# Kernel optimization log

Measured on AMD Instinct MI355X. Metric: run time of the kernel, lower is better.

## Reference

```python
import jax, jax.numpy as jnp
import numpy as np

B, C, H, W = 4, 1024, 14, 14
L = 80          # num labels / graph nodes
WD = 300        # word embedding dim
INTER = 1024    # semantic intermediary dim
OUT = 2048      # output_dim
TIME_STEP = 3


def setup_inputs() -> dict:
    key = jax.random.key(0)
    ks = jax.random.split(key, 24)
    s = 0.02  # weight scale to keep gates/tanh in sane range
    return {
        "img_feature_map": jax.random.normal(ks[0], (B, C, H, W), jnp.float32),
        "word_embedding": jax.random.normal(ks[1], (L, WD), jnp.float32),
        "adjacency": jax.random.uniform(ks[2], (L, L), jnp.float32) / L,
        "fc1_w": jax.random.normal(ks[3], (INTER, C), jnp.float32) * s,
        "fc2_w": jax.random.normal(ks[4], (INTER, WD), jnp.float32) * s,
        "fc3_w": jax.random.normal(ks[5], (INTER, INTER), jnp.float32) * s,
        "fc3_b": jnp.zeros((INTER,), jnp.float32),
        "fca_w": jax.random.normal(ks[6], (1, INTER), jnp.float32) * s,
        "fca_b": jnp.zeros((1,), jnp.float32),
        "w3": jax.random.normal(ks[7], (C, 2 * C), jnp.float32) * s,
        "b3": jnp.zeros((C,), jnp.float32),
        "u3": jax.random.normal(ks[8], (C, C), jnp.float32) * s,
        "u3b": jnp.zeros((C,), jnp.float32),
        "w4": jax.random.normal(ks[9], (C, 2 * C), jnp.float32) * s,
        "b4": jnp.zeros((C,), jnp.float32),
        "w5": jax.random.normal(ks[10], (C, 2 * C), jnp.float32) * s,
        "b5": jnp.zeros((C,), jnp.float32),
        "u5": jax.random.normal(ks[11], (C, C), jnp.float32) * s,
        "u5b": jnp.zeros((C,), jnp.float32),
        "fco_w": jax.random.normal(ks[12], (OUT, 2 * C), jnp.float32) * s,
        "fco_b": jnp.zeros((OUT,), jnp.float32),
    }


def _semantic(fmap, word_emb, fc1_w, fc2_w, fc3_w, fc3_b, fca_w, fca_b):
    # Faithful to torch: view(-1, C) on a contiguous (B,C,H,W) tensor is a raw
    # row-major reinterpret (NOT a BHWC transpose). jnp.reshape matches.
    b, c, h, w = fmap.shape
    x = fmap.reshape(-1, c)                                   # (B*H*W, C)
    f_wh = x @ fc1_w.T                                        # (N, INTER)
    f_wd = word_emb @ fc2_w.T                                 # (L, INTER)
    lb = jnp.tanh(f_wh[:, None, :] * f_wd[None, :, :])        # (N, L, INTER)
    lb = lb @ fc3_w.T + fc3_b                                 # (N, L, INTER)
    coeff = lb @ fca_w.T + fca_b                              # (N, L, 1)
    coeff = coeff.reshape(b, L, h * w)                        # torch .view semantics
    coeff = jax.nn.softmax(coeff, axis=2)
    coeff = coeff.reshape(b, h, w, L)
    fmap_bhwc = fmap.reshape(b, h, w, c)                      # raw reinterpret, as torch
    return jnp.einsum('bhwl,bhwc->blc', coeff, fmap_bhwc)     # (B, L, C)


def _ggnn(nodes, adj, w3, b3, u3, u3b, w4, b4, w5, b5, u5, u5b):
    for _ in range(TIME_STEP):
        a = jnp.einsum('nm,bmd->bnd', adj, nodes)             # in == out matrix
        av = jnp.concatenate([a, a], axis=-1)                 # (B, L, 2C)
        u3x = nodes @ u3.T + u3b
        z = jax.nn.sigmoid(av @ w3.T + b3 + u3x)
        r = jax.nn.sigmoid(av @ w4.T + b4 + u3x)              # torch bug: reuses fc_eq3_u
        hcand = jnp.tanh(av @ w5.T + b5 + (r * nodes) @ u5.T + u5b)
        nodes = (1.0 - z) * nodes + z * hcand
    return nodes


def reference(img_feature_map, word_embedding, adjacency,
              fc1_w, fc2_w, fc3_w, fc3_b, fca_w, fca_b,
              w3, b3, u3, u3b, w4, b4, w5, b5, u5, u5b,
              fco_w, fco_b):
    g = _semantic(img_feature_map, word_embedding,
                  fc1_w, fc2_w, fc3_w, fc3_b, fca_w, fca_b)   # (B, L, C)
    nodes = _ggnn(g, adjacency, w3, b3, u3, u3b, w4, b4, w5, b5, u5, u5b)
    feat = jnp.concatenate([nodes, g], axis=-1)               # (B, L, 2C)
    out = jnp.tanh(feat @ fco_w.T + fco_b)                    # (B, L, OUT)
    return out
```

## Files before the change

### kernel.cpp

```cpp
#include <hip/hip_runtime.h>
#include <hip/hip_bf16.h>

#define LL 80
#define NPIX 784
#define PBATCH 15680

#define DI __device__ __forceinline__

typedef short s8v __attribute__((ext_vector_type(8)));
typedef short short4v __attribute__((ext_vector_type(4)));
typedef float f32x4 __attribute__((ext_vector_type(4)));

DI float b2f(__hip_bfloat16 x) { return __bfloat162float(x); }
DI float s2f(short h) { return __uint_as_float(((unsigned int)(unsigned short)h) << 16); }

DI short f2b(float x) {
    unsigned int b = __float_as_uint(x);
    b += 0x7fffu + ((b >> 16) & 1u);
    return (short)(b >> 16);
}

template <int F> DI float LD(const void* p, int i) {
    if (F) return ((const float*)p)[i];
    return b2f(((const __hip_bfloat16*)p)[i]);
}
DI float LDf(int f, const void* p, int i) { return f ? ((const float*)p)[i] : b2f(((const __hip_bfloat16*)p)[i]); }

DI float fast_tanh(float x) {
    float e = __expf(2.0f * x);
    return 1.0f - 2.0f / (e + 1.0f);
}
DI float fast_sigmoid(float x) { return 1.0f / (1.0f + __expf(-x)); }

__global__ __launch_bounds__(256) void detect_dtype(const void* probe, int n, int* flag) {
    __shared__ int bad;
    if (threadIdx.x == 0) bad = 0;
    __syncthreads();
    int c = 0;
    for (int i = threadIdx.x; i < n; i += 256) {
        float v = b2f(((const __hip_bfloat16*)probe)[i]);
        if (!(fabsf(v) < 1000.0f)) c++;
    }
    if (c) atomicAdd(&bad, c);
    __syncthreads();
    if (threadIdx.x == 0) *flag = (bad > 8) ? 1 : 0;
}

DI void cvt_part(int f, const void* src, short* __restrict__ dst, int blk, int n) {
    int i0 = (blk * 256 + threadIdx.x) * 4;
    if (i0 >= n) return;
    if (f) {
        float4 v = *(const float4*)((const float*)src + i0);
        short4v o = { f2b(v.x), f2b(v.y), f2b(v.z), f2b(v.w) };
        *(short4v*)(dst + i0) = o;
    } else {
        *(short4v*)(dst + i0) = *(const short4v*)((const short*)src + i0);
    }
}

DI void wcat_part(int f, const void* w3, const void* w4, const void* w5, const void* u3,
                  short* __restrict__ wcat, int blk) {
    int i0 = (blk * 256 + threadIdx.x) * 4;
    int nr = i0 >> 10, k = i0 & 1023;
    int j = nr >> 10, r = nr & 1023;
    const void* W = (j == 0) ? w3 : (j == 1) ? w4 : (j == 2) ? w5 : u3;
    float4 v;
    if (j < 3) {
        if (f) {
            float4 x = *(const float4*)((const float*)W + r * 2048 + k);
            float4 y = *(const float4*)((const float*)W + r * 2048 + 1024 + k);
            v.x = x.x + y.x; v.y = x.y + y.y; v.z = x.z + y.z; v.w = x.w + y.w;
        } else {
            const short* Ws = (const short*)W;
            short4v x = *(const short4v*)(Ws + r * 2048 + k);
            short4v y = *(const short4v*)(Ws + r * 2048 + 1024 + k);
            v.x = s2f(x.x) + s2f(y.x); v.y = s2f(x.y) + s2f(y.y);
            v.z = s2f(x.z) + s2f(y.z); v.w = s2f(x.w) + s2f(y.w);
        }
    } else {
        if (f) v = *(const float4*)((const float*)W + r * 1024 + k);
        else {
            short4v x = *(const short4v*)((const short*)W + r * 1024 + k);
            v.x = s2f(x.x); v.y = s2f(x.y); v.z = s2f(x.z); v.w = s2f(x.w);
        }
    }
    short4v o = { f2b(v.x), f2b(v.y), f2b(v.z), f2b(v.w) };
    *(short4v*)(wcat + i0) = o;
}

template <int F>
DI void u_part(const void* fc3_w, const void* fca_w, float* __restrict__ uP, int jsplit) {
    int k4 = threadIdx.x * 4;
    float4 acc = {0.f, 0.f, 0.f, 0.f};
    for (int j = jsplit * 16; j < jsplit * 16 + 16; j++) {
        float fa = LD<F>(fca_w, j);
        float4 row;
        if (F) row = *(const float4*)((const float*)fc3_w + j * 1024 + k4);
        else {
            short4v x = *(const short4v*)((const short*)fc3_w + j * 1024 + k4);
            row.x = s2f(x.x); row.y = s2f(x.y); row.z = s2f(x.z); row.w = s2f(x.w);
        }
        acc.x += fa * row.x; acc.y += fa * row.y;
        acc.z += fa * row.z; acc.w += fa * row.w;
    }
    *(float4*)(uP + jsplit * 1024 + k4) = acc;
}

template <int F>
DI void c0_part(const void* fc3_b, const void* fca_w, const void* fca_b,
                float* c0, float* red) {
    float acc = 0.f;
    for (int j = threadIdx.x; j < 1024; j += 256)
        acc += LD<F>(fc3_b, j) * LD<F>(fca_w, j);
    red[threadIdx.x] = acc;
    __syncthreads();
    for (int s = 128; s > 0; s >>= 1) {
        if (threadIdx.x < s) red[threadIdx.x] += red[threadIdx.x + s];
        __syncthreads();
    }
    if (threadIdx.x == 0) *c0 = red[0] + LD<F>(fca_b, 0);
}

template <int F>
DI void fc2_part(float* lds, const void* word, const void* fc2_w, float* C,
                 int bx, int by, int kb, int ke) {
    float* As = lds;
    float* Ws2 = lds + 1088;
    const int tid = threadIdx.x;
    const int tx = tid & 15, ty = tid >> 4;
    const int m0 = by * 64, n0 = bx * 64;
    const int M = 80;
    float acc[4][4] = {};

    for (int k0 = kb; k0 < ke; k0 += 16) {
#pragma unroll
        for (int i = 0; i < 4; i++) {
            int idx = tid + i * 256;
            int kk = idx & 15, mm = idx >> 4;
            int m = m0 + mm, k = k0 + kk;
            As[kk * 68 + mm] = (m < M && k < ke) ? LD<F>(word, m * 300 + k) : 0.f;
        }
#pragma unroll
        for (int i = 0; i < 4; i++) {
            int idx = tid + i * 256;
            int kk = idx & 15, nn = idx >> 4;
            int n = n0 + nn, k = k0 + kk;
            Ws2[kk * 68 + nn] = (k < ke) ? LD<F>(fc2_w, n * 300 + k) : 0.f;
        }
        __syncthreads();
#pragma unroll
        for (int kk = 0; kk < 16; kk++) {
            float4 av = *(const float4*)(&As[kk * 68 + ty * 4]);
            float4 wv = *(const float4*)(&Ws2[kk * 68 + tx * 4]);
            float a4[4] = {av.x, av.y, av.z, av.w};
            float w4[4] = {wv.x, wv.y, wv.z, wv.w};
#pragma unroll
            for (int i = 0; i < 4; i++)
#pragma unroll
                for (int j = 0; j < 4; j++)
                    acc[i][j] += a4[i] * w4[j];
        }
        __syncthreads();
    }

    for (int i = 0; i < 4; i++) {
        int m = m0 + ty * 4 + i;
        if (m >= M) continue;
        for (int j = 0; j < 4; j++)
            C[m * 1024 + n0 + tx * 4 + j] = acc[i][j];
    }
}

__global__ __launch_bounds__(256) void mega_prep(
    const int* flag,
    const void* fmap, const void* fc1_w, const void* u5w, const void* fco_w,
    const void* w3, const void* w4, const void* w5, const void* u3,
    const void* fc3_w, const void* fc3_b, const void* fca_w, const void* fca_b,
    const void* word, const void* fc2_w,
    short* fmap_b, short* fc1w_b, short* u5w_b, short* wcat_b, short* fcow_b,
    float* uP, float* c0, float* f_wdP) {
    __shared__ float lds[2176];
    int f = *flag;
    int bid = blockIdx.x;
    if (bid < 64) {
        if (f) u_part<1>(fc3_w, fca_w, uP, bid);
        else   u_part<0>(fc3_w, fca_w, uP, bid);
    } else if (bid == 64) {
        if (f) c0_part<1>(fc3_b, fca_w, fca_b, c0, lds);
        else   c0_part<0>(fc3_b, fca_w, fca_b, c0, lds);
    } else if (bid < 193) {
        int r = bid - 65;
        int sp = r >> 5, rr = r & 31;
        int kb = sp * 80, ke = (sp == 3) ? 300 : kb + 80;
        float* C = f_wdP + sp * 81920;
        if (f) fc2_part<1>(lds, word, fc2_w, C, rr & 15, rr >> 4, kb, ke);
        else   fc2_part<0>(lds, word, fc2_w, C, rr & 15, rr >> 4, kb, ke);
    }
    else if (bid < 977)  cvt_part(f, fmap,  fmap_b, bid - 193,  802816);
    else if (bid < 2001) cvt_part(f, fc1_w, fc1w_b, bid - 977,  1048576);
    else if (bid < 3025) cvt_part(f, u5w,   u5w_b,  bid - 2001, 1048576);
    else if (bid < 7121) wcat_part(f, w3, w4, w5, u3, wcat_b, bid - 3025);
    else                 cvt_part(f, fco_w, fcow_b, bid - 7121, 4194304);
}

__global__ __launch_bounds__(256) void reduce_pre(
    const float* __restrict__ uP, const float* __restrict__ f_wdP,
    float* __restrict__ u, float* __restrict__ f_wd) {
    if (blockIdx.x < 80) {
        int i4 = (blockIdx.x * 256 + threadIdx.x) * 4;
        float4 a = *(const float4*)(f_wdP + i4);
        float4 b = *(const float4*)(f_wdP + 81920 + i4);
        float4 c = *(const float4*)(f_wdP + 163840 + i4);
        float4 d = *(const float4*)(f_wdP + 245760 + i4);
        float4 o = {a.x+b.x+c.x+d.x, a.y+b.y+c.y+d.y, a.z+b.z+c.z+d.z, a.w+b.w+c.w+d.w};
        *(float4*)(f_wd + i4) = o;
    } else {
        int k4 = threadIdx.x * 4;
        float4 acc = {0.f, 0.f, 0.f, 0.f};
        for (int p = 0; p < 64; p++) {
            float4 q = *(const float4*)(uP + p * 1024 + k4);
            acc.x += q.x; acc.y += q.y; acc.z += q.z; acc.w += q.w;
        }
        *(float4*)(u + k4) = acc;
    }
}

DI void mcore_b(const short* __restrict__ A, int lda,
                const short* __restrict__ B, int ldb,
                float* __restrict__ C, int ldc,
                int M, int kb, int ke, int m0, int n0) {
    __shared__ short As[4][64][8];
    __shared__ short Ws[4][64][8];
    const int tid = threadIdx.x;
    const int wv = tid >> 6, lane = tid & 63;
    const int mA = tid & 63, qA = tid >> 6;
    const int gm = m0 + mA;
    const int lp = (mA & 15) | (qA << 4), lg = mA >> 4;
    f32x4 acc[4] = {};

    s8v va = {0,0,0,0,0,0,0,0};
    if (gm < M) va = *(const s8v*)(A + gm * lda + kb + 8 * qA);
    s8v vb = *(const s8v*)(B + (n0 + mA) * ldb + kb + 8 * qA);

    for (int k0 = kb; k0 < ke; k0 += 32) {
        *(s8v*)&As[lg][lp][0] = va;
        *(s8v*)&Ws[lg][lp][0] = vb;
        __syncthreads();
        int kn = k0 + 32;
        if (kn < ke) {
            if (gm < M) va = *(const s8v*)(A + gm * lda + kn + 8 * qA);
            vb = *(const s8v*)(B + (n0 + mA) * ldb + kn + 8 * qA);
        }
        s8v af = *(const s8v*)&As[wv][lane][0];
#pragma unroll
        for (int nf = 0; nf < 4; nf++) {
            s8v bf = *(const s8v*)&Ws[nf][lane][0];
            acc[nf] = __builtin_amdgcn_mfma_f32_16x16x32_bf16(af, bf, acc[nf], 0, 0, 0);
        }
        __syncthreads();
    }

    const int q = lane >> 4, cc = lane & 15;
#pragma unroll
    for (int nf = 0; nf < 4; nf++) {
        int n = n0 + 16 * nf + cc;
#pragma unroll
        for (int r = 0; r < 4; r++) {
            int m = m0 + 16 * wv + q * 4 + r;
            if (m < M) C[m * ldc + n] = acc[nf][r];
        }
    }
}

__global__ __launch_bounds__(256) void mfma_fc1(
    const short* __restrict__ fmap_b, const short* __restrict__ fc1w_b,
    float* __restrict__ fhP) {
    int z = blockIdx.z;
    mcore_b(fmap_b, 1024, fc1w_b, 1024, fhP + z * 802816, 1024,
            NPIX, z * 512, z * 512 + 512, blockIdx.y * 64, blockIdx.x * 64);
}

__global__ __launch_bounds__(256) void mfma_gate(
    const short* __restrict__ a_b, const short* __restrict__ nodes_b,
    const short* __restrict__ wcat_b, float* __restrict__ gP) {
    int z = blockIdx.z;
    const short* A = (blockIdx.x >= 48) ? nodes_b : a_b;
    mcore_b(A, 1024, wcat_b, 1024, gP + z * 1310720, 4096,
            320, z * 512, z * 512 + 512, blockIdx.y * 64, blockIdx.x * 64);
}

__global__ __launch_bounds__(256) void mfma_u5f(
    const int* flag, const short* __restrict__ rn_b, const short* __restrict__ u5w_b,
    const float* __restrict__ gP,
    const void* b3, const void* u3b, const void* b5, const void* u5b,
    float* __restrict__ nodes, short* __restrict__ nodes_b) {
    __shared__ short As[4][64][8];
    __shared__ short Ws[4][64][8];
    const int tid = threadIdx.x;
    const int wv = tid >> 6, lane = tid & 63;
    const int mA = tid & 63, qA = tid >> 6;
    const int lp = (mA & 15) | (qA << 4), lg = mA >> 4;
    const int m0 = blockIdx.y * 64, n0 = blockIdx.x * 64;
    f32x4 acc[4] = {};

    s8v va = *(const s8v*)(rn_b + (m0 + mA) * 1024 + 8 * qA);
    s8v vb = *(const s8v*)(u5w_b + (n0 + mA) * 1024 + 8 * qA);

    for (int k0 = 0; k0 < 1024; k0 += 32) {
        *(s8v*)&As[lg][lp][0] = va;
        *(s8v*)&Ws[lg][lp][0] = vb;
        __syncthreads();
        int kn = k0 + 32;
        if (kn < 1024) {
            va = *(const s8v*)(rn_b + (m0 + mA) * 1024 + kn + 8 * qA);
            vb = *(const s8v*)(u5w_b + (n0 + mA) * 1024 + kn + 8 * qA);
        }
        s8v af = *(const s8v*)&As[wv][lane][0];
#pragma unroll
        for (int nf = 0; nf < 4; nf++) {
            s8v bf = *(const s8v*)&Ws[nf][lane][0];
            acc[nf] = __builtin_amdgcn_mfma_f32_16x16x32_bf16(af, bf, acc[nf], 0, 0, 0);
        }
        __syncthreads();
    }

    const int f = *flag;
    const int q = lane >> 4, cc = lane & 15;
#pragma unroll
    for (int nf = 0; nf < 4; nf++) {
        int n = n0 + 16 * nf + cc;
        float bb3 = LDf(f, b3, n), bu3 = LDf(f, u3b, n);
        float bb5 = LDf(f, b5, n), bu5 = LDf(f, u5b, n);
#pragma unroll
        for (int r = 0; r < 4; r++) {
            int m = m0 + 16 * wv + q * 4 + r;
            int i = m * 1024 + n, base = m * 4096;
            float az = gP[base + n]        + gP[1310720 + base + n];
            float ah = gP[base + 2048 + n] + gP[1310720 + base + 2048 + n];
            float ux = gP[base + 3072 + n] + gP[1310720 + base + 3072 + n];
            float z = fast_sigmoid(az + ux + bb3 + bu3);
            float h = fast_tanh(ah + acc[nf][r] + bb5 + bu5);
            float nd = (1.f - z) * nodes[i] + z * h;
            nodes[i] = nd;
            nodes_b[i] = f2b(nd);
        }
    }
}

__global__ __launch_bounds__(256) void mfma_finf(
    const int* flag, const short* __restrict__ nodes_b, const short* __restrict__ g_b,
    const short* __restrict__ fcow_b, const void* fco_b, void* out) {
    __shared__ short As[4][64][8];
    __shared__ short Ws[4][64][8];
    const int tid = threadIdx.x;
    const int wv = tid >> 6, lane = tid & 63;
    const int mA = tid & 63, qA = tid >> 6;
    const int lp = (mA & 15) | (qA << 4), lg = mA >> 4;
    const int m0 = blockIdx.y * 64, n0 = blockIdx.x * 64;
    f32x4 acc[4] = {};

    s8v va = *(const s8v*)(nodes_b + (m0 + mA) * 1024 + 8 * qA);
    s8v vb = *(const s8v*)(fcow_b + (n0 + mA) * 2048 + 8 * qA);

    for (int k0 = 0; k0 < 2048; k0 += 32) {
        *(s8v*)&As[lg][lp][0] = va;
        *(s8v*)&Ws[lg][lp][0] = vb;
        __syncthreads();
        int kn = k0 + 32;
        if (kn < 2048) {
            const short* Apn = (kn < 1024) ? nodes_b : (g_b - 1024);
            va = *(const s8v*)(Apn + (m0 + mA) * 1024 + kn + 8 * qA);
            vb = *(const s8v*)(fcow_b + (n0 + mA) * 2048 + kn + 8 * qA);
        }
        s8v af = *(const s8v*)&As[wv][lane][0];
#pragma unroll
        for (int nf = 0; nf < 4; nf++) {
            s8v bf = *(const s8v*)&Ws[nf][lane][0];
            acc[nf] = __builtin_amdgcn_mfma_f32_16x16x32_bf16(af, bf, acc[nf], 0, 0, 0);
        }
        __syncthreads();
    }

    const int f = *flag;
    const int q = lane >> 4, cc = lane & 15;
#pragma unroll
    for (int nf = 0; nf < 4; nf++) {
        int n = n0 + 16 * nf + cc;
        float bias = LDf(f, fco_b, n);
#pragma unroll
        for (int r = 0; r < 4; r++) {
            int m = m0 + 16 * wv + q * 4 + r;
            float v = fast_tanh(acc[nf][r] + bias);
            if (f) ((float*)out)[m * 2048 + n] = v;
            else   ((__hip_bfloat16*)out)[m * 2048 + n] = __float2bfloat16(v);
        }
    }
}

__global__ __launch_bounds__(256) void coeff_kernel(
    const float* __restrict__ fhP, const float* __restrict__ f_wd,
    const float* __restrict__ u, const float* __restrict__ c0p,
    float* __restrict__ s) {
    int n = blockIdx.x;
    __shared__ float4 fh4[256];
    __shared__ float4 uu4[256];
    int t = threadIdx.x;
    {
        float4 a0 = *(const float4*)(fhP + n * 1024 + t * 4);
        float4 a1 = *(const float4*)(fhP + 802816 + n * 1024 + t * 4);
        float4 fv = {a0.x + a1.x, a0.y + a1.y, a0.z + a1.z, a0.w + a1.w};
        fh4[t] = fv;
        uu4[t] = *(const float4*)(u + t * 4);
    }
    __syncthreads();
    float c0 = *c0p;
    int wave = t >> 6, lane = t & 63;
    int b = n / 196, hw = n % 196;
    int l0 = blockIdx.y * 40;
    for (int l = l0 + wave; l < l0 + 40; l += 4) {
        const float4* fd4 = (const float4*)(f_wd + l * 1024);
        float p = 0.f;
#pragma unroll
        for (int k = 0; k < 4; k++) {
            int idx = lane + k * 64;
            float4 h = fh4[idx];
            float4 d = fd4[idx];
            float4 uu = uu4[idx];
            p += fast_tanh(h.x * d.x) * uu.x;
            p += fast_tanh(h.y * d.y) * uu.y;
            p += fast_tanh(h.z * d.z) * uu.z;
            p += fast_tanh(h.w * d.w) * uu.w;
        }
        for (int off = 32; off > 0; off >>= 1) p += __shfl_down(p, off);
        if (lane == 0) s[b * PBATCH + hw * LL + l] = p + c0;
    }
}

__global__ __launch_bounds__(64) void softmax196(float* __restrict__ s) {
    float* p = s + blockIdx.x * 196;
    int lane = threadIdx.x;
    float v[4];
    float mx = -1e30f;
#pragma unroll
    for (int i = 0; i < 4; i++) {
        int idx = lane + i * 64;
        v[i] = (idx < 196) ? p[idx] : -1e30f;
        mx = fmaxf(mx, v[i]);
    }
    for (int off = 32; off > 0; off >>= 1) mx = fmaxf(mx, __shfl_down(mx, off));
    mx = __shfl(mx, 0);
    float sum = 0.f;
#pragma unroll
    for (int i = 0; i < 4; i++) {
        int idx = lane + i * 64;
        if (idx < 196) { v[i] = __expf(v[i] - mx); sum += v[i]; }
    }
    for (int off = 32; off > 0; off >>= 1) sum += __shfl_down(sum, off);
    sum = __shfl(sum, 0);
    float inv = 1.f / sum;
#pragma unroll
    for (int i = 0; i < 4; i++) {
        int idx = lane + i * 64;
        if (idx < 196) p[idx] = v[i] * inv;
    }
}

__global__ __launch_bounds__(256) void g_kernel(
    const float* __restrict__ s, const short* __restrict__ fmap_b,
    float* __restrict__ nodes, short* __restrict__ nodes_b, short* __restrict__ g_b) {
    int bl = blockIdx.x;
    int b = bl / LL, l = bl % LL;
    __shared__ float co[196];
    for (int i = threadIdx.x; i < 196; i += 256)
        co[i] = s[b * PBATCH + i * LL + l];
    __syncthreads();
    int c4 = threadIdx.x * 4;
    const short* base = fmap_b + b * 196 * 1024 + c4;
    float a0 = 0.f, a1 = 0.f, a2 = 0.f, a3 = 0.f;
    for (int hw = 0; hw < 196; hw++) {
        short4v v = *(const short4v*)(base + hw * 1024);
        float w = co[hw];
        a0 += w * s2f(v.x); a1 += w * s2f(v.y);
        a2 += w * s2f(v.z); a3 += w * s2f(v.w);
    }
    int o = bl * 1024 + c4;
    float4 fa = {a0, a1, a2, a3};
    *(float4*)(nodes + o) = fa;
    short4v bb = { f2b(a0), f2b(a1), f2b(a2), f2b(a3) };
    *(short4v*)(nodes_b + o) = bb;
    *(short4v*)(g_b + o) = bb;
}

template <int F>
DI void adj_core(float* arw, const void* adj, const float* nodes, short* a_b) {
    int bl = blockIdx.x;
    int b = bl / LL, l = bl % LL;
    if (threadIdx.x < LL) arw[threadIdx.x] = LD<F>(adj, l * LL + threadIdx.x);
    __syncthreads();
    int c4 = threadIdx.x * 4;
    const float* nb = nodes + b * LL * 1024 + c4;
    float a0 = 0.f, a1 = 0.f, a2 = 0.f, a3 = 0.f;
    for (int m = 0; m < LL; m++) {
        float am = arw[m];
        float4 nd = *(const float4*)(nb + m * 1024);
        a0 += am * nd.x; a1 += am * nd.y; a2 += am * nd.z; a3 += am * nd.w;
    }
    short4v bb = { f2b(a0), f2b(a1), f2b(a2), f2b(a3) };
    *(short4v*)(a_b + bl * 1024 + c4) = bb;
}

__global__ __launch_bounds__(256) void adj_kernel(
    const int* flag, const void* adj, const float* nodes, short* a_b) {
    __shared__ float arw[LL];
    if (*flag) adj_core<1>(arw, adj, nodes, a_b);
    else       adj_core<0>(arw, adj, nodes, a_b);
}

template <int F>
DI void ew_r_core(const float* gP, const float* nodes,
                  const void* b4, const void* u3b, short* rn_b, int i4) {
    int m = i4 >> 10, c = i4 & 1023;
    int base = m * 4096;
    float4 r0 = *(const float4*)(gP + base + 1024 + c);
    float4 r1 = *(const float4*)(gP + 1310720 + base + 1024 + c);
    float4 x0 = *(const float4*)(gP + base + 3072 + c);
    float4 x1 = *(const float4*)(gP + 1310720 + base + 3072 + c);
    float4 nd = *(const float4*)(nodes + i4);
    short4v o;
    o.x = f2b(fast_sigmoid(r0.x + r1.x + x0.x + x1.x + LD<F>(b4, c)   + LD<F>(u3b, c))   * nd.x);
    o.y = f2b(fast_sigmoid(r0.y + r1.y + x0.y + x1.y + LD<F>(b4, c+1) + LD<F>(u3b, c+1)) * nd.y);
    o.z = f2b(fast_sigmoid(r0.z + r1.z + x0.z + x1.z + LD<F>(b4, c+2) + LD<F>(u3b, c+2)) * nd.z);
    o.w = f2b(fast_sigmoid(r0.w + r1.w + x0.w + x1.w + LD<F>(b4, c+3) + LD<F>(u3b, c+3)) * nd.w);
    *(short4v*)(rn_b + i4) = o;
}

__global__ void ew_r(const int* flag, const float* gP, const float* nodes,
                     const void* b4, const void* u3b, short* rn_b, int n) {
    int i4 = (blockIdx.x * 256 + threadIdx.x) * 4;
    if (i4 >= n) return;
    if (*flag) ew_r_core<1>(gP, nodes, b4, u3b, rn_b, i4);
    else       ew_r_core<0>(gP, nodes, b4, u3b, rn_b, i4);
}

extern "C" void kernel_launch(void* const* d_in, const int* in_sizes, int n_in,
                              void* d_out, int out_size, void* d_ws, size_t ws_size,
                              hipStream_t stream) {
    const void* fmap  = d_in[0];
    const void* word  = d_in[1];
    const void* adjm  = d_in[2];
    const void* fc1_w = d_in[3];
    const void* fc2_w = d_in[4];
    const void* fc3_w = d_in[5];
    const void* fc3_b = d_in[6];
    const void* fca_w = d_in[7];
    const void* fca_b = d_in[8];
    const void* w3    = d_in[9];
    const void* b3    = d_in[10];
    const void* u3    = d_in[11];
    const void* u3b   = d_in[12];
    const void* w4    = d_in[13];
    const void* b4    = d_in[14];
    const void* w5    = d_in[15];
    const void* b5    = d_in[16];
    const void* u5    = d_in[17];
    const void* u5b   = d_in[18];
    const void* fco_w = d_in[19];
    const void* fco_b = d_in[20];

    int*   flag    = (int*)d_ws;
    float* P       = (float*)d_ws + 16;
    float* nodes   = P;                       P += 327680;
    short* nodes_b = (short*)P;               P += 163840;
    short* g_b     = (short*)P;               P += 163840;
    short* a_b     = (short*)P;               P += 163840;
    short* rn_b    = (short*)P;               P += 163840;
    short* u5w_b   = (short*)P;               P += 524288;
    short* wcat_b  = (short*)P;               P += 2097152;
    float* R       = P;
    float* fhP    = R;
    float* f_wd   = R + 1605632;
    float* f_wdP  = f_wd + 81920;
    float* uP     = f_wdP + 327680;
    float* u      = uP + 65536;
    float* c0     = u + 1024;
    float* s      = c0 + 16;
    short* fmap_b = (short*)(s + 62720);
    short* fc1w_b = (short*)(s + 62720 + 401408);
    short* fcow_b = (short*)(R + 3070224);
    float* gP     = R;

    detect_dtype<<<1, 256, 0, stream>>>(fc1_w, 4096, flag);

    mega_prep<<<11217, 256, 0, stream>>>(flag, fmap, fc1_w, u5, fco_w,
                                         w3, w4, w5, u3,
                                         fc3_w, fc3_b, fca_w, fca_b,
                                         word, fc2_w,
                                         fmap_b, fc1w_b, u5w_b, wcat_b, fcow_b,
                                         uP, c0, f_wdP);
    reduce_pre<<<81, 256, 0, stream>>>(uP, f_wdP, u, f_wd);

    mfma_fc1<<<dim3(16, 13, 2), 256, 0, stream>>>(fmap_b, fc1w_b, fhP);
    coeff_kernel<<<dim3(NPIX, 2), 256, 0, stream>>>(fhP, f_wd, u, c0, s);
    softmax196<<<320, 64, 0, stream>>>(s);
    g_kernel<<<320, 256, 0, stream>>>(s, fmap_b, nodes, nodes_b, g_b);

    for (int t = 0; t < 3; t++) {
        adj_kernel<<<320, 256, 0, stream>>>(flag, adjm, nodes, a_b);
        mfma_gate<<<dim3(64, 5, 2), 256, 0, stream>>>(a_b, nodes_b, wcat_b, gP);
        ew_r<<<320, 256, 0, stream>>>(flag, gP, nodes, b4, u3b, rn_b, 327680);
        mfma_u5f<<<dim3(16, 5), 256, 0, stream>>>(flag, rn_b, u5w_b, gP,
                                                  b3, u3b, b5, u5b, nodes, nodes_b);
    }

    mfma_finf<<<dim3(32, 5), 256, 0, stream>>>(flag, nodes_b, g_b, fcow_b, fco_b, d_out);
}
```

Measured before the change: 394.5 us.

## Reassociate adjacency after gate GEMM, fuse reductions into fc1, rewrite coeff tanh

New measurement: 395.3 us. About the same (+0.2%).

```diff
diff --git a/kernel.cpp b/kernel.cpp
--- a/kernel.cpp
+++ b/kernel.cpp
@@ -203,28 +203,6 @@
     else                 cvt_part(f, fco_w, fcow_b, bid - 7121, 4194304);
 }
 
-__global__ __launch_bounds__(256) void reduce_pre(
-    const float* __restrict__ uP, const float* __restrict__ f_wdP,
-    float* __restrict__ u, float* __restrict__ f_wd) {
-    if (blockIdx.x < 80) {
-        int i4 = (blockIdx.x * 256 + threadIdx.x) * 4;
-        float4 a = *(const float4*)(f_wdP + i4);
-        float4 b = *(const float4*)(f_wdP + 81920 + i4);
-        float4 c = *(const float4*)(f_wdP + 163840 + i4);
-        float4 d = *(const float4*)(f_wdP + 245760 + i4);
-        float4 o = {a.x+b.x+c.x+d.x, a.y+b.y+c.y+d.y, a.z+b.z+c.z+d.z, a.w+b.w+c.w+d.w};
-        *(float4*)(f_wd + i4) = o;
-    } else {
-        int k4 = threadIdx.x * 4;
-        float4 acc = {0.f, 0.f, 0.f, 0.f};
-        for (int p = 0; p < 64; p++) {
-            float4 q = *(const float4*)(uP + p * 1024 + k4);
-            acc.x += q.x; acc.y += q.y; acc.z += q.z; acc.w += q.w;
-        }
-        *(float4*)(u + k4) = acc;
-    }
-}
-
 DI void mcore_b(const short* __restrict__ A, int lda,
                 const short* __restrict__ B, int ldb,
                 float* __restrict__ C, int ldc,
@@ -272,26 +250,120 @@
     }
 }
 
-__global__ __launch_bounds__(256) void mfma_fc1(
+__global__ __launch_bounds__(256) void fc1_plus(
     const short* __restrict__ fmap_b, const short* __restrict__ fc1w_b,
-    float* __restrict__ fhP) {
+    float* __restrict__ fhP,
+    const float* __restrict__ uP, const float* __restrict__ f_wdP,
+    float* __restrict__ u, float* __restrict__ f_wd,
+    const float* __restrict__ c0, float* __restrict__ sc) {
+    int bid = blockIdx.x;
+    if (bid < 416) {
+        int z = bid / 208, rem = bid % 208;
+        mcore_b(fmap_b, 1024, fc1w_b, 1024, fhP + z * 802816, 1024,
+                NPIX, z * 512, z * 512 + 512, (rem / 16) * 64, (rem % 16) * 64);
+    } else if (bid < 496) {
+        int i4 = ((bid - 416) * 256 + threadIdx.x) * 4;
+        float4 a = *(const float4*)(f_wdP + i4);
+        float4 b = *(const float4*)(f_wdP + 81920 + i4);
+        float4 c = *(const float4*)(f_wdP + 163840 + i4);
+        float4 d = *(const float4*)(f_wdP + 245760 + i4);
+        float4 o = {a.x+b.x+c.x+d.x, a.y+b.y+c.y+d.y, a.z+b.z+c.z+d.z, a.w+b.w+c.w+d.w};
+        *(float4*)(f_wd + i4) = o;
+    } else {
+        __shared__ float red[256];
+        int t = threadIdx.x;
+        int k4 = t * 4;
+        float4 acc = {0.f, 0.f, 0.f, 0.f};
+        for (int p = 0; p < 64; p++) {
+            float4 q = *(const float4*)(uP + p * 1024 + k4);
+            acc.x += q.x; acc.y += q.y; acc.z += q.z; acc.w += q.w;
+        }
+        *(float4*)(u + k4) = acc;
+        red[t] = acc.x + acc.y + acc.z + acc.w;
+        __syncthreads();
+        for (int s2 = 128; s2 > 0; s2 >>= 1) {
+            if (t < s2) red[t] += red[t + s2];
+            __syncthreads();
+        }
+        if (t == 0) *sc = red[0] + *c0;
+    }
+}
+
+__global__ __launch_bounds__(256) void mfma_nw(
+    const short* __restrict__ nodes_b, const short* __restrict__ wcat_b,
+    float* __restrict__ nwP) {
     int z = blockIdx.z;
-    mcore_b(fmap_b, 1024, fc1w_b, 1024, fhP + z * 802816, 1024,
-            NPIX, z * 512, z * 512 + 512, blockIdx.y * 64, blockIdx.x * 64);
-}
-
-__global__ __launch_bounds__(256) void mfma_gate(
-    const short* __restrict__ a_b, const short* __restrict__ nodes_b,
-    const short* __restrict__ wcat_b, float* __restrict__ gP) {
-    int z = blockIdx.z;
-    const short* A = (blockIdx.x >= 48) ? nodes_b : a_b;
-    mcore_b(A, 1024, wcat_b, 1024, gP + z * 1310720, 4096,
+    mcore_b(nodes_b, 1024, wcat_b, 1024, nwP + z * 1310720, 4096,
             320, z * 512, z * 512 + 512, blockIdx.y * 64, blockIdx.x * 64);
+}
+
+__global__ __launch_bounds__(256) void mix_kernel(
+    const int* flag, const void* adjm, const float* __restrict__ nwP,
+    const float* __restrict__ nodes, const void* b4, const void* u3b,
+    float* __restrict__ gPm, short* __restrict__ rn_b) {
+    __shared__ float adjL[6400];
+    __shared__ float tile[5120];
+    __shared__ float t2[5120];
+    int bid = blockIdx.x;
+    int b = bid / 48, ct = bid % 48;
+    int t = threadIdx.x;
+    int f = *flag;
+    for (int i = t; i < 6400; i += 256) adjL[i] = LDf(f, adjm, i);
+    int reg = ct >> 4;
+    int cb = (ct & 15) * 64;
+    int srcc = reg * 1024 + cb;
+    for (int i = t; i < 1280; i += 256) {
+        int m = i >> 4, c4 = (i & 15) * 4;
+        const float* p0 = nwP + (size_t)(b * 80 + m) * 4096 + srcc + c4;
+        float4 x = *(const float4*)p0;
+        float4 y = *(const float4*)(p0 + 1310720);
+        float4 v = {x.x + y.x, x.y + y.y, x.z + y.z, x.w + y.w};
+        *(float4*)&tile[m * 64 + c4] = v;
+    }
+    if (reg == 1) {
+        for (int i = t; i < 1280; i += 256) {
+            int m = i >> 4, c4 = (i & 15) * 4;
+            const float* p0 = nwP + (size_t)(b * 80 + m) * 4096 + 3072 + cb + c4;
+            float4 x = *(const float4*)p0;
+            float4 y = *(const float4*)(p0 + 1310720);
+            float4 v = {x.x + y.x, x.y + y.y, x.z + y.z, x.w + y.w};
+            *(float4*)&t2[m * 64 + c4] = v;
+        }
+    }
+    __syncthreads();
+    int wv = t >> 6, lane = t & 63;
+    float acc[20];
+#pragma unroll
+    for (int p = 0; p < 20; p++) acc[p] = 0.f;
+    for (int m = 0; m < 80; m++) {
+        float tv = tile[m * 64 + lane];
+#pragma unroll
+        for (int p = 0; p < 20; p++)
+            acc[p] += adjL[(wv + 4 * p) * 80 + m] * tv;
+    }
+    if (reg == 1) {
+        int cg = cb + lane;
+        float bb = LDf(f, b4, cg) + LDf(f, u3b, cg);
+#pragma unroll
+        for (int p = 0; p < 20; p++) {
+            int l = wv + 4 * p;
+            int bl = b * 80 + l;
+            float r = fast_sigmoid(acc[p] + t2[l * 64 + lane] + bb);
+            rn_b[bl * 1024 + cg] = f2b(r * nodes[bl * 1024 + cg]);
+        }
+    } else {
+        int off = (reg == 0) ? 0 : 1024;
+#pragma unroll
+        for (int p = 0; p < 20; p++) {
+            int bl = b * 80 + wv + 4 * p;
+            gPm[bl * 2048 + off + cb + lane] = acc[p];
+        }
+    }
 }
 
 __global__ __launch_bounds__(256) void mfma_u5f(
     const int* flag, const short* __restrict__ rn_b, const short* __restrict__ u5w_b,
-    const float* __restrict__ gP,
+    const float* __restrict__ gPm, const float* __restrict__ nwP,
     const void* b3, const void* u3b, const void* b5, const void* u5b,
     float* __restrict__ nodes, short* __restrict__ nodes_b) {
     __shared__ short As[4][64][8];
@@ -329,17 +401,18 @@
 #pragma unroll
     for (int nf = 0; nf < 4; nf++) {
         int n = n0 + 16 * nf + cc;
-        float bb3 = LDf(f, b3, n), bu3 = LDf(f, u3b, n);
-        float bb5 = LDf(f, b5, n), bu5 = LDf(f, u5b, n);
+        float bb3 = LDf(f, b3, n) + LDf(f, u3b, n);
+        float bb5 = LDf(f, b5, n) + LDf(f, u5b, n);
 #pragma unroll
         for (int r = 0; r < 4; r++) {
             int m = m0 + 16 * wv + q * 4 + r;
-            int i = m * 1024 + n, base = m * 4096;
-            float az = gP[base + n]        + gP[1310720 + base + n];
-            float ah = gP[base + 2048 + n] + gP[1310720 + base + 2048 + n];
-            float ux = gP[base + 3072 + n] + gP[1310720 + base + 3072 + n];
-            float z = fast_sigmoid(az + ux + bb3 + bu3);
-            float h = fast_tanh(ah + acc[nf][r] + bb5 + bu5);
+            int i = m * 1024 + n;
+            float az = gPm[m * 2048 + n];
+            float ah = gPm[m * 2048 + 1024 + n];
+            const float* up = nwP + (size_t)m * 4096 + 3072 + n;
+            float ux = up[0] + up[1310720];
+            float z = fast_sigmoid(az + ux + bb3);
+            float h = fast_tanh(ah + acc[nf][r] + bb5);
             float nd = (1.f - z) * nodes[i] + z * h;
             nodes[i] = nd;
             nodes_b[i] = f2b(nd);
@@ -399,7 +472,7 @@
 
 __global__ __launch_bounds__(256) void coeff_kernel(
     const float* __restrict__ fhP, const float* __restrict__ f_wd,
-    const float* __restrict__ u, const float* __restrict__ c0p,
+    const float* __restrict__ u, const float* __restrict__ scp,
     float* __restrict__ s) {
     int n = blockIdx.x;
     __shared__ float4 fh4[256];
@@ -408,16 +481,16 @@
     {
         float4 a0 = *(const float4*)(fhP + n * 1024 + t * 4);
         float4 a1 = *(const float4*)(fhP + 802816 + n * 1024 + t * 4);
-        float4 fv = {a0.x + a1.x, a0.y + a1.y, a0.z + a1.z, a0.w + a1.w};
+        float4 fv = {2.f*(a0.x + a1.x), 2.f*(a0.y + a1.y), 2.f*(a0.z + a1.z), 2.f*(a0.w + a1.w)};
         fh4[t] = fv;
         uu4[t] = *(const float4*)(u + t * 4);
     }
     __syncthreads();
-    float c0 = *c0p;
+    float sc = *scp;
     int wave = t >> 6, lane = t & 63;
     int b = n / 196, hw = n % 196;
-    int l0 = blockIdx.y * 40;
-    for (int l = l0 + wave; l < l0 + 40; l += 4) {
+    int l0 = blockIdx.y * 20;
+    for (int l = l0 + wave; l < l0 + 20; l += 4) {
         const float4* fd4 = (const float4*)(f_wd + l * 1024);
         float p = 0.f;
 #pragma unroll
@@ -426,13 +499,13 @@
             float4 h = fh4[idx];
             float4 d = fd4[idx];
             float4 uu = uu4[idx];
-            p += fast_tanh(h.x * d.x) * uu.x;
-            p += fast_tanh(h.y * d.y) * uu.y;
-            p += fast_tanh(h.z * d.z) * uu.z;
-            p += fast_tanh(h.w * d.w) * uu.w;
+            p += uu.x * __builtin_amdgcn_rcpf(__expf(h.x * d.x) + 1.f);
+            p += uu.y * __builtin_amdgcn_rcpf(__expf(h.y * d.y) + 1.f);
+            p += uu.z * __builtin_amdgcn_rcpf(__expf(h.z * d.z) + 1.f);
+            p += uu.w * __builtin_amdgcn_rcpf(__expf(h.w * d.w) + 1.f);
         }
         for (int off = 32; off > 0; off >>= 1) p += __shfl_down(p, off);
-        if (lane == 0) s[b * PBATCH + hw * LL + l] = p + c0;
+        if (lane == 0) s[b * PBATCH + hw * LL + l] = sc - 2.f * p;
     }
 }
 
@@ -489,57 +562,6 @@
     short4v bb = { f2b(a0), f2b(a1), f2b(a2), f2b(a3) };
     *(short4v*)(nodes_b + o) = bb;
     *(short4v*)(g_b + o) = bb;
-}
-
-template <int F>
-DI void adj_core(float* arw, const void* adj, const float* nodes, short* a_b) {
-    int bl = blockIdx.x;
-    int b = bl / LL, l = bl % LL;
-    if (threadIdx.x < LL) arw[threadIdx.x] = LD<F>(adj, l * LL + threadIdx.x);
-    __syncthreads();
-    int c4 = threadIdx.x * 4;
-    const float* nb = nodes + b * LL * 1024 + c4;
-    float a0 = 0.f, a1 = 0.f, a2 = 0.f, a3 = 0.f;
-    for (int m = 0; m < LL; m++) {
-        float am = arw[m];
-        float4 nd = *(const float4*)(nb + m * 1024);
-        a0 += am * nd.x; a1 += am * nd.y; a2 += am * nd.z; a3 += am * nd.w;
-    }
-    short4v bb = { f2b(a0), f2b(a1), f2b(a2), f2b(a3) };
-    *(short4v*)(a_b + bl * 1024 + c4) = bb;
-}
-
-__global__ __launch_bounds__(256) void adj_kernel(
-    const int* flag, const void* adj, const float* nodes, short* a_b) {
-    __shared__ float arw[LL];
-    if (*flag) adj_core<1>(arw, adj, nodes, a_b);
-    else       adj_core<0>(arw, adj, nodes, a_b);
-}
-
-template <int F>
-DI void ew_r_core(const float* gP, const float* nodes,
-                  const void* b4, const void* u3b, short* rn_b, int i4) {
-    int m = i4 >> 10, c = i4 & 1023;
-    int base = m * 4096;
-    float4 r0 = *(const float4*)(gP + base + 1024 + c);
-    float4 r1 = *(const float4*)(gP + 1310720 + base + 1024 + c);
-    float4 x0 = *(const float4*)(gP + base + 3072 + c);
-    float4 x1 = *(const float4*)(gP + 1310720 + base + 3072 + c);
-    float4 nd = *(const float4*)(nodes + i4);
-    short4v o;
-    o.x = f2b(fast_sigmoid(r0.x + r1.x + x0.x + x1.x + LD<F>(b4, c)   + LD<F>(u3b, c))   * nd.x);
-    o.y = f2b(fast_sigmoid(r0.y + r1.y + x0.y + x1.y + LD<F>(b4, c+1) + LD<F>(u3b, c+1)) * nd.y);
-    o.z = f2b(fast_sigmoid(r0.z + r1.z + x0.z + x1.z + LD<F>(b4, c+2) + LD<F>(u3b, c+2)) * nd.z);
-    o.w = f2b(fast_sigmoid(r0.w + r1.w + x0.w + x1.w + LD<F>(b4, c+3) + LD<F>(u3b, c+3)) * nd.w);
-    *(short4v*)(rn_b + i4) = o;
-}
-
-__global__ void ew_r(const int* flag, const float* gP, const float* nodes,
-                     const void* b4, const void* u3b, short* rn_b, int n) {
-    int i4 = (blockIdx.x * 256 + threadIdx.x) * 4;
-    if (i4 >= n) return;
-    if (*flag) ew_r_core<1>(gP, nodes, b4, u3b, rn_b, i4);
-    else       ew_r_core<0>(gP, nodes, b4, u3b, rn_b, i4);
 }
 
 extern "C" void kernel_launch(void* const* d_in, const int* in_sizes, int n_in,
@@ -572,7 +594,6 @@
     float* nodes   = P;                       P += 327680;
     short* nodes_b = (short*)P;               P += 163840;
     short* g_b     = (short*)P;               P += 163840;
-    short* a_b     = (short*)P;               P += 163840;
     short* rn_b    = (short*)P;               P += 163840;
     short* u5w_b   = (short*)P;               P += 524288;
     short* wcat_b  = (short*)P;               P += 2097152;
@@ -583,11 +604,13 @@
     float* uP     = f_wdP + 327680;
     float* u      = uP + 65536;
     float* c0     = u + 1024;
-    float* s      = c0 + 16;
+    float* sc     = c0 + 16;
+    float* s      = sc + 16;
     short* fmap_b = (short*)(s + 62720);
     short* fc1w_b = (short*)(s + 62720 + 401408);
-    short* fcow_b = (short*)(R + 3070224);
-    float* gP     = R;
+    float* nwP    = R;
+    float* gPm    = R + 2621440;
+    short* fcow_b = (short*)(R + 3276800);
 
     detect_dtype<<<1, 256, 0, stream>>>(fc1_w, 4096, flag);
 
@@ -597,18 +620,16 @@
                                          word, fc2_w,
                                          fmap_b, fc1w_b, u5w_b, wcat_b, fcow_b,
                                          uP, c0, f_wdP);
-    reduce_pre<<<81, 256, 0, stream>>>(uP, f_wdP, u, f_wd);
-
-    mfma_fc1<<<dim3(16, 13, 2), 256, 0, stream>>>(fmap_b, fc1w_b, fhP);
-    coeff_kernel<<<dim3(NPIX, 2), 256, 0, stream>>>(fhP, f_wd, u, c0, s);
+
+    fc1_plus<<<497, 256, 0, stream>>>(fmap_b, fc1w_b, fhP, uP, f_wdP, u, f_wd, c0, sc);
+    coeff_kernel<<<dim3(NPIX, 4), 256, 0, stream>>>(fhP, f_wd, u, sc, s);
     softmax196<<<320, 64, 0, stream>>>(s);
     g_kernel<<<320, 256, 0, stream>>>(s, fmap_b, nodes, nodes_b, g_b);
 
     for (int t = 0; t < 3; t++) {
-        adj_kernel<<<320, 256, 0, stream>>>(flag, adjm, nodes, a_b);
-        mfma_gate<<<dim3(64, 5, 2), 256, 0, stream>>>(a_b, nodes_b, wcat_b, gP);
-        ew_r<<<320, 256, 0, stream>>>(flag, gP, nodes, b4, u3b, rn_b, 327680);
-        mfma_u5f<<<dim3(16, 5), 256, 0, stream>>>(flag, rn_b, u5w_b, gP,
+        mfma_nw<<<dim3(64, 5, 2), 256, 0, stream>>>(nodes_b, wcat_b, nwP);
+        mix_kernel<<<192, 256, 0, stream>>>(flag, adjm, nwP, nodes, b4, u3b, gPm, rn_b);
+        mfma_u5f<<<dim3(16, 5), 256, 0, stream>>>(flag, rn_b, u5w_b, gPm, nwP,
                                                   b3, u3b, b5, u5b, nodes, nodes_b);
     }
 
```
